# Kernel optimization log

Hardware: AMD Instinct MI355X
Metric: run time of the kernel (lower is better)

The kernel has to match this reference:

```python
import jax, jax.numpy as jnp
import numpy as np

B, CH, D, H, W = 2, 1, 10, 512, 512
BONUS = 10.0
EPS = 1e-7

C_, L_, R_ = slice(1, -1), slice(0, -2), slice(2, None)


def setup_inputs() -> dict:
    key = jax.random.key(0)
    x = jax.random.normal(key, (B, CH, D, H, W), dtype=jnp.float32)
    return {"x": x}


def _pad_rep(x):
    # replicate ('edge') padding of 1 on D,H,W, as kornia spatial_gradient3d / nms3d
    return jnp.pad(x, ((0, 0), (0, 0), (1, 1), (1, 1), (1, 1)), mode='edge')


def _forward(x, bonus=BONUS, eps=EPS):
    Dd, Hh, Ww = x.shape[-3:]
    xp = _pad_rep(x)

    # --- first-order central differences (spatial_gradient3d, mode='diff', order=1) ---
    gx = 0.5 * (xp[:, :, C_, C_, R_] - xp[:, :, C_, C_, L_])
    gy = 0.5 * (xp[:, :, C_, R_, C_] - xp[:, :, C_, L_, C_])
    gs = 0.5 * (xp[:, :, R_, C_, C_] - xp[:, :, L_, C_, C_])

    # --- second-order finite differences (order=2); cross terms scaled by 0.25 (OpenCV convention) ---
    cc = xp[:, :, C_, C_, C_]
    dxx = xp[:, :, C_, C_, L_] + xp[:, :, C_, C_, R_] - 2.0 * cc
    dyy = xp[:, :, C_, L_, C_] + xp[:, :, C_, R_, C_] - 2.0 * cc
    dss = xp[:, :, L_, C_, C_] + xp[:, :, R_, C_, C_] - 2.0 * cc
    dxy = 0.25 * (xp[:, :, C_, L_, L_] + xp[:, :, C_, R_, R_] - xp[:, :, C_, R_, L_] - xp[:, :, C_, L_, R_])
    dys = 0.25 * (xp[:, :, L_, L_, C_] + xp[:, :, R_, R_, C_] - xp[:, :, R_, L_, C_] - xp[:, :, L_, R_, C_])
    dxs = 0.25 * (xp[:, :, L_, C_, L_] + xp[:, :, R_, C_, R_] - xp[:, :, R_, C_, L_] - xp[:, :, L_, C_, R_])

    # --- strict 3x3x3 NMS: x must exceed all 26 neighbors AND 0 (kornia zeroed-center kernel) ---
    nmax = None
    for dz in range(3):
        for dyo in range(3):
            for dxo in range(3):
                if dz == 1 and dyo == 1 and dxo == 1:
                    continue
                v = xp[:, :, dz:dz + Dd, dyo:dyo + Hh, dxo:dxo + Ww]
                nmax = v if nmax is None else jnp.maximum(nmax, v)
    nmax = jnp.maximum(nmax, jnp.zeros((), x.dtype))
    m = x > nmax  # strict local maxima mask (B,CH,D,H,W)

    # --- per-voxel 3x3 solve H dx = b via Cramer's rule, only at maxima ---
    # torch adds a fixed small random |U(0,1)|*eps matrix to every Hessian to avoid singularity
    Rm = jax.random.uniform(jax.random.key(42), (3, 3), dtype=x.dtype) * eps

    ident = [[1.0, 0.0, 0.0], [0.0, 1.0, 0.0], [0.0, 0.0, 1.0]]

    def sel(h, i, j):
        # masked voxels get identity Hessian -> zero solution, safe division, clean grads
        return jnp.where(m, h + Rm[i, j], jnp.asarray(ident[i][j], x.dtype))

    h00 = sel(dxx, 0, 0); h01 = sel(dxy, 0, 1); h02 = sel(dxs, 0, 2)
    h10 = sel(dxy, 1, 0); h11 = sel(dyy, 1, 1); h12 = sel(dys, 1, 2)
    h20 = sel(dxs, 2, 0); h21 = sel(dys, 2, 1); h22 = sel(dss, 2, 2)
    z = jnp.zeros((), x.dtype)
    b0 = jnp.where(m, gx, z); b1 = jnp.where(m, gy, z); b2 = jnp.where(m, gs, z)

    c00 = h11 * h22 - h12 * h21
    c01 = h10 * h22 - h12 * h20
    c02 = h10 * h21 - h11 * h20
    det = h00 * c00 - h01 * c01 + h02 * c02
    sx = (b0 * c00 - h01 * (b1 * h22 - h12 * b2) + h02 * (b1 * h21 - h11 * b2)) / det
    sy = (h00 * (b1 * h22 - h12 * b2) - b0 * c01 + h02 * (h10 * b2 - b1 * h20)) / det
    ss = (h00 * (h11 * b2 - h21 * b1) - h01 * (h10 * b2 - h20 * b1) + b0 * c02) / det

    dx0, dx1, dx2 = -sx, -sy, -ss  # subpixel offsets (x, y, scale)

    # discard offsets far from the window center (>0.7)
    far = jnp.maximum(jnp.maximum(jnp.abs(dx0), jnp.abs(dx1)), jnp.abs(dx2)) > 0.7
    dx0 = jnp.where(far, z, dx0); dx1 = jnp.where(far, z, dx1); dx2 = jnp.where(far, z, dx2)

    # refined peak value: y = x + 0.5 * b^T dx, plus strict-maxima bonus
    dy_ = 0.5 * (gx * dx0 + gy * dx1 + gs * dx2)
    y_max = x + dy_ + bonus * m.astype(x.dtype)

    # global coordinates + subpixel offsets, channel order (scale/d, y, x)
    gd = jnp.arange(Dd, dtype=x.dtype)[:, None, None]
    gh = jnp.arange(Hh, dtype=x.dtype)[None, :, None]
    gw = jnp.arange(Ww, dtype=x.dtype)[None, None, :]
    coords_max = jnp.stack([gd + dx2, gh + dx1, gw + dx0], axis=2)  # (B,CH,3,D,H,W)
    return coords_max, y_max


def reference(x):
    return _forward(x, BONUS, EPS)
```

## Files before the change

kernel.cpp:

```cpp
#include <hip/hip_runtime.h>


constexpr int Dd = 10, Hh = 512, Ww = 512;
constexpr int HW  = Hh * Ww;
constexpr int DHW = Dd * HW;
constexpr float BONUS_F = 10.0f;

__global__ __launch_bounds__(256) void quad_kernel(
        const float* __restrict__ x, float* __restrict__ out) {
    const int tx = threadIdx.x;
    const int w  = (blockIdx.x << 6) + tx;
    const int h0 = (blockIdx.y << 3) + (threadIdx.y << 1);
    const int bd = blockIdx.z;
    const int d  = bd % Dd;
    const int b  = bd / Dd;

    const int wm = (w == 0) ? 0 : w - 1,      wp = (w == Ww - 1) ? w : w + 1;
    const int zm = (d == 0) ? bd : bd - 1,    zp = (d == Dd - 1) ? bd : bd + 1;
    const int hr[4] = { (h0 == 0) ? 0 : h0 - 1, h0, h0 + 1,
                        (h0 + 2 > Hh - 1) ? Hh - 1 : h0 + 2 };
    const int zz[3] = { zm, bd, zp };

    float L[3][4], C[3][4], R[3][4];
#pragma unroll
    for (int z = 0; z < 3; ++z) {
        const float* pl = x + (size_t)zz[z] * HW;
#pragma unroll
        for (int r = 0; r < 4; ++r) {
            const float* rp = pl + (size_t)hr[r] * Ww;
            L[z][r] = rp[wm];
            C[z][r] = rp[w];
            R[z][r] = rp[wp];
        }
    }

    float sh = 0.0f;
#pragma unroll
    for (int z = 0; z < 3; ++z)
#pragma unroll
        for (int r = 1; r <= 2; ++r) {
            sh = fmaxf(sh, L[z][r]);
            sh = fmaxf(sh, R[z][r]);
            if (z != 1) sh = fmaxf(sh, C[z][r]);
        }

#pragma unroll
    for (int o = 0; o < 2; ++o) {
        const int r0 = o, r1 = o + 1, r2 = o + 2;
        const float xc = C[1][r1];

        const int rx = (o == 0) ? 0 : 3;
        float nm = sh;
#pragma unroll
        for (int z = 0; z < 3; ++z) {
            nm = fmaxf(nm, L[z][rx]);
            nm = fmaxf(nm, C[z][rx]);
            nm = fmaxf(nm, R[z][rx]);
        }
        nm = fmaxf(nm, C[1][(o == 0) ? 2 : 1]);
        const bool m = xc > nm;

        const float gx  = 0.5f * (R[1][r1] - L[1][r1]);
        const float gy  = 0.5f * (C[1][r2] - C[1][r0]);
        const float gs  = 0.5f * (C[2][r1] - C[0][r1]);
        const float dxx = L[1][r1] + R[1][r1] - 2.0f * xc;
        const float dyy = C[1][r0] + C[1][r2] - 2.0f * xc;
        const float dss = C[0][r1] + C[2][r1] - 2.0f * xc;
        const float dxy = 0.25f * (L[1][r0] + R[1][r2] - L[1][r2] - R[1][r0]);
        const float dys = 0.25f * (C[0][r0] + C[2][r2] - C[2][r0] - C[0][r2]);
        const float dxs = 0.25f * (L[0][r1] + R[2][r1] - L[2][r1] - R[0][r1]);

        const float c00 = dyy * dss - dys * dys;
        const float c01 = dxy * dss - dys * dxs;
        const float c02 = dxy * dys - dyy * dxs;
        const float det = dxx * c00 - dxy * c01 + dxs * c02;
        const float t1  = gy * dss - dys * gs;
        const float t2  = gy * dys - dyy * gs;
        const float t3  = dxy * gs - gy * dxs;
        const float nx  = gx * c00 - dxy * t1 + dxs * t2;
        const float ny  = dxx * t1 - gx * c01 + dxs * t3;
        const float ns  = dxx * (-t2) - dxy * t3 + gx * c02;

        const float lim = 0.7f * fabsf(det);
        const bool keep = m && (fabsf(det) > 0.0f) &&
                          (fabsf(nx) <= lim) && (fabsf(ny) <= lim) && (fabsf(ns) <= lim);
        const float rdet = keep ? (1.0f / det) : 0.0f;
        const float dx0 = -nx * rdet;
        const float dx1 = -ny * rdet;
        const float dx2 = -ns * rdet;

        const float dy_ = 0.5f * (gx * dx0 + gy * dx1 + gs * dx2);
        const float y   = xc + dy_ + (m ? BONUS_F : 0.0f);

        const size_t idx = (size_t)d * HW + (size_t)(h0 + o) * Ww + w;
        out[((size_t)(b * 3 + 0)) * DHW + idx] = (float)d + dx2;
        out[((size_t)(b * 3 + 1)) * DHW + idx] = (float)(h0 + o) + dx1;
        out[((size_t)(b * 3 + 2)) * DHW + idx] = (float)w + dx0;
        out[(size_t)6 * DHW + (size_t)b * DHW + idx] = y;
    }
}

extern "C" void kernel_launch(void* const* d_in, const int* in_sizes, int n_in,
                              void* d_out, int out_size, void* d_ws, size_t ws_size,
                              hipStream_t stream) {
    (void)in_sizes; (void)n_in; (void)out_size; (void)d_ws; (void)ws_size;
    const float* x = (const float*)d_in[0];
    float* out = (float*)d_out;
    dim3 block(64, 4, 1);
    dim3 grid(Ww / 64, Hh / 8, 2 * Dd);
    quad_kernel<<<grid, block, 0, stream>>>(x, out);
}
```

Before: 108.1 us.

## Process four W-columns per thread with float4 loads, stores, and shared NMS maxima

Each thread now handles a 4-wide strip of columns by 2 rows, loading each stencil row as one float4 plus two scalar halo values, and writing all four outputs as float4 stores. NMS neighbour maxima are factored into per-row 3-wide column maxima that adjacent voxels reuse. This cuts redundant neighbour loads and the number of memory instructions per output. In exchange, register pressure rises and the grid drops to a quarter as many blocks (2560), which lowers parallelism.

```diff
diff --git a/kernel.cpp b/kernel.cpp
--- a/kernel.cpp
+++ b/kernel.cpp
@@ -9,94 +9,112 @@
 __global__ __launch_bounds__(256) void quad_kernel(
         const float* __restrict__ x, float* __restrict__ out) {
     const int tx = threadIdx.x;
-    const int w  = (blockIdx.x << 6) + tx;
+    const int w0 = (blockIdx.x << 8) + (tx << 2);
     const int h0 = (blockIdx.y << 3) + (threadIdx.y << 1);
     const int bd = blockIdx.z;
     const int d  = bd % Dd;
     const int b  = bd / Dd;
 
-    const int wm = (w == 0) ? 0 : w - 1,      wp = (w == Ww - 1) ? w : w + 1;
-    const int zm = (d == 0) ? bd : bd - 1,    zp = (d == Dd - 1) ? bd : bd + 1;
+    const int wl = (w0 == 0) ? 0 : w0 - 1;
+    const int wr = (w0 + 4 > Ww - 1) ? Ww - 1 : w0 + 4;
+    const int zm = (d == 0) ? bd : bd - 1, zp = (d == Dd - 1) ? bd : bd + 1;
     const int hr[4] = { (h0 == 0) ? 0 : h0 - 1, h0, h0 + 1,
                         (h0 + 2 > Hh - 1) ? Hh - 1 : h0 + 2 };
     const int zz[3] = { zm, bd, zp };
 
-    float L[3][4], C[3][4], R[3][4];
+    float V[3][4][6];
 #pragma unroll
     for (int z = 0; z < 3; ++z) {
         const float* pl = x + (size_t)zz[z] * HW;
 #pragma unroll
         for (int r = 0; r < 4; ++r) {
             const float* rp = pl + (size_t)hr[r] * Ww;
-            L[z][r] = rp[wm];
-            C[z][r] = rp[w];
-            R[z][r] = rp[wp];
+            const float4 v4 = *reinterpret_cast<const float4*>(rp + w0);
+            V[z][r][0] = rp[wl];
+            V[z][r][1] = v4.x;  V[z][r][2] = v4.y;
+            V[z][r][3] = v4.z;  V[z][r][4] = v4.w;
+            V[z][r][5] = rp[wr];
         }
     }
 
-    float sh = 0.0f;
+    float zc[4][4], pm2[2][4];
 #pragma unroll
-    for (int z = 0; z < 3; ++z)
+    for (int r = 0; r < 4; ++r)
 #pragma unroll
-        for (int r = 1; r <= 2; ++r) {
-            sh = fmaxf(sh, L[z][r]);
-            sh = fmaxf(sh, R[z][r]);
-            if (z != 1) sh = fmaxf(sh, C[z][r]);
+        for (int j = 0; j < 4; ++j) {
+            const float c0 = fmaxf(fmaxf(V[0][r][j], V[0][r][j+1]), V[0][r][j+2]);
+            const float c1 = fmaxf(fmaxf(V[1][r][j], V[1][r][j+1]), V[1][r][j+2]);
+            const float c2 = fmaxf(fmaxf(V[2][r][j], V[2][r][j+1]), V[2][r][j+2]);
+            zc[r][j] = fmaxf(fmaxf(c0, c1), c2);
+            if (r == 1 || r == 2) {
+                const float lr = fmaxf(V[1][r][j], V[1][r][j+2]);
+                pm2[r-1][j] = fmaxf(fmaxf(c0, c2), lr);
+            }
         }
 
 #pragma unroll
     for (int o = 0; o < 2; ++o) {
         const int r0 = o, r1 = o + 1, r2 = o + 2;
-        const float xc = C[1][r1];
+        float rd[4], rh[4], rw[4], ry[4];
 
-        const int rx = (o == 0) ? 0 : 3;
-        float nm = sh;
 #pragma unroll
-        for (int z = 0; z < 3; ++z) {
-            nm = fmaxf(nm, L[z][rx]);
-            nm = fmaxf(nm, C[z][rx]);
-            nm = fmaxf(nm, R[z][rx]);
+        for (int j = 0; j < 4; ++j) {
+            const float xc = V[1][r1][j+1];
+
+            const float nm = fmaxf(
+                fmaxf(fmaxf(zc[r0][j], zc[r2][j]), pm2[r1-1][j]), 0.0f);
+            const bool m = xc > nm;
+
+            const float gx  = 0.5f * (V[1][r1][j+2] - V[1][r1][j]);
+            const float gy  = 0.5f * (V[1][r2][j+1] - V[1][r0][j+1]);
+            const float gs  = 0.5f * (V[2][r1][j+1] - V[0][r1][j+1]);
+            const float dxx = V[1][r1][j]   + V[1][r1][j+2] - 2.0f * xc;
+            const float dyy = V[1][r0][j+1] + V[1][r2][j+1] - 2.0f * xc;
+            const float dss = V[0][r1][j+1] + V[2][r1][j+1] - 2.0f * xc;
+            const float dxy = 0.25f * (V[1][r0][j]   + V[1][r2][j+2]
+                                     - V[1][r2][j]   - V[1][r0][j+2]);
+            const float dys = 0.25f * (V[0][r0][j+1] + V[2][r2][j+1]
+                                     - V[2][r0][j+1] - V[0][r2][j+1]);
+            const float dxs = 0.25f * (V[0][r1][j]   + V[2][r1][j+2]
+                                     - V[2][r1][j]   - V[0][r1][j+2]);
+
+            const float c00 = dyy * dss - dys * dys;
+            const float c01 = dxy * dss - dys * dxs;
+            const float c02 = dxy * dys - dyy * dxs;
+            const float det = dxx * c00 - dxy * c01 + dxs * c02;
+            const float t1  = gy * dss - dys * gs;
+            const float t2  = gy * dys - dyy * gs;
+            const float t3  = dxy * gs - gy * dxs;
+            const float nx  = gx * c00 - dxy * t1 + dxs * t2;
+            const float ny  = dxx * t1 - gx * c01 + dxs * t3;
+            const float ns  = dxx * (-t2) - dxy * t3 + gx * c02;
+
+            const float lim = 0.7f * fabsf(det);
+            const bool keep = m && (fabsf(det) > 0.0f) &&
+                              (fabsf(nx) <= lim) && (fabsf(ny) <= lim) &&
+                              (fabsf(ns) <= lim);
+            const float rdet = keep ? (1.0f / det) : 0.0f;
+            const float dx0 = -nx * rdet;
+            const float dx1 = -ny * rdet;
+            const float dx2 = -ns * rdet;
+
+            const float dy_ = 0.5f * (gx * dx0 + gy * dx1 + gs * dx2);
+
+            rd[j] = (float)d + dx2;
+            rh[j] = (float)(h0 + o) + dx1;
+            rw[j] = (float)(w0 + j) + dx0;
+            ry[j] = xc + dy_ + (m ? BONUS_F : 0.0f);
         }
-        nm = fmaxf(nm, C[1][(o == 0) ? 2 : 1]);
-        const bool m = xc > nm;
 
-        const float gx  = 0.5f * (R[1][r1] - L[1][r1]);
-        const float gy  = 0.5f * (C[1][r2] - C[1][r0]);
-        const float gs  = 0.5f * (C[2][r1] - C[0][r1]);
-        const float dxx = L[1][r1] + R[1][r1] - 2.0f * xc;
-        const float dyy = C[1][r0] + C[1][r2] - 2.0f * xc;
-        const float dss = C[0][r1] + C[2][r1] - 2.0f * xc;
-        const float dxy = 0.25f * (L[1][r0] + R[1][r2] - L[1][r2] - R[1][r0]);
-        const float dys = 0.25f * (C[0][r0] + C[2][r2] - C[2][r0] - C[0][r2]);
-        const float dxs = 0.25f * (L[0][r1] + R[2][r1] - L[2][r1] - R[0][r1]);
-
-        const float c00 = dyy * dss - dys * dys;
-        const float c01 = dxy * dss - dys * dxs;
-        const float c02 = dxy * dys - dyy * dxs;
-        const float det = dxx * c00 - dxy * c01 + dxs * c02;
-        const float t1  = gy * dss - dys * gs;
-        const float t2  = gy * dys - dyy * gs;
-        const float t3  = dxy * gs - gy * dxs;
-        const float nx  = gx * c00 - dxy * t1 + dxs * t2;
-        const float ny  = dxx * t1 - gx * c01 + dxs * t3;
-        const float ns  = dxx * (-t2) - dxy * t3 + gx * c02;
-
-        const float lim = 0.7f * fabsf(det);
-        const bool keep = m && (fabsf(det) > 0.0f) &&
-                          (fabsf(nx) <= lim) && (fabsf(ny) <= lim) && (fabsf(ns) <= lim);
-        const float rdet = keep ? (1.0f / det) : 0.0f;
-        const float dx0 = -nx * rdet;
-        const float dx1 = -ny * rdet;
-        const float dx2 = -ns * rdet;
-
-        const float dy_ = 0.5f * (gx * dx0 + gy * dx1 + gs * dx2);
-        const float y   = xc + dy_ + (m ? BONUS_F : 0.0f);
-
-        const size_t idx = (size_t)d * HW + (size_t)(h0 + o) * Ww + w;
-        out[((size_t)(b * 3 + 0)) * DHW + idx] = (float)d + dx2;
-        out[((size_t)(b * 3 + 1)) * DHW + idx] = (float)(h0 + o) + dx1;
-        out[((size_t)(b * 3 + 2)) * DHW + idx] = (float)w + dx0;
-        out[(size_t)6 * DHW + (size_t)b * DHW + idx] = y;
+        const size_t idx = (size_t)d * HW + (size_t)(h0 + o) * Ww + w0;
+        *reinterpret_cast<float4*>(out + ((size_t)(b * 3 + 0)) * DHW + idx) =
+            make_float4(rd[0], rd[1], rd[2], rd[3]);
+        *reinterpret_cast<float4*>(out + ((size_t)(b * 3 + 1)) * DHW + idx) =
+            make_float4(rh[0], rh[1], rh[2], rh[3]);
+        *reinterpret_cast<float4*>(out + ((size_t)(b * 3 + 2)) * DHW + idx) =
+            make_float4(rw[0], rw[1], rw[2], rw[3]);
+        *reinterpret_cast<float4*>(out + (size_t)6 * DHW + (size_t)b * DHW + idx) =
+            make_float4(ry[0], ry[1], ry[2], ry[3]);
     }
 }
 
@@ -107,6 +125,6 @@
     const float* x = (const float*)d_in[0];
     float* out = (float*)d_out;
     dim3 block(64, 4, 1);
-    dim3 grid(Ww / 64, Hh / 8, 2 * Dd);
+    dim3 grid(Ww / 256, Hh / 8, 2 * Dd);
     quad_kernel<<<grid, block, 0, stream>>>(x, out);
 }
```

After: 108.8 us, median of 2. No clear change (+0.7%).
